# Kernel tuning notes

Measured on AMD Instinct MI355X. Metric: run time of the kernel, lower is better.

Reference implementation:

```python
import jax, jax.numpy as jnp
import numpy as np

DEPTH, HEADS, DIM_HEAD = 6, 12, 64
DIM, MLP, FEAT = 768, 3072, 1000
B, N = 32, 196
EPS = 1e-5


def layernorm(x, g, b):
    m = jnp.mean(x, axis=-1, keepdims=True)
    v = jnp.var(x, axis=-1, keepdims=True)
    return (x - m) * jax.lax.rsqrt(v + EPS) * g + b


def setup_inputs() -> dict:
    key = jax.random.key(0)
    ks = jax.random.split(key, 8)
    s = 0.02
    return {
        "x": jax.random.normal(ks[0], (B, N, DIM), jnp.float32),
        "cls_token": jax.random.normal(ks[1], (1, 1, DIM), jnp.float32),
        "ln1_g": jnp.ones((DEPTH, DIM), jnp.float32),
        "ln1_b": jnp.zeros((DEPTH, DIM), jnp.float32),
        "w_qkv": jax.random.normal(ks[2], (DEPTH, DIM, 3 * HEADS * DIM_HEAD), jnp.float32) * s,
        "reattn_w": jax.random.normal(ks[3], (DEPTH, HEADS, HEADS), jnp.float32),
        "reattn_g": jnp.ones((DEPTH, HEADS), jnp.float32),
        "reattn_b": jnp.zeros((DEPTH, HEADS), jnp.float32),
        "w_out": jax.random.normal(ks[4], (DEPTH, HEADS * DIM_HEAD, DIM), jnp.float32) * s,
        "b_out": jnp.zeros((DEPTH, DIM), jnp.float32),
        "ln2_g": jnp.ones((DEPTH, DIM), jnp.float32),
        "ln2_b": jnp.zeros((DEPTH, DIM), jnp.float32),
        "w1": jax.random.normal(ks[5], (DEPTH, DIM, MLP), jnp.float32) * s,
        "b1": jnp.zeros((DEPTH, MLP), jnp.float32),
        "w2": jax.random.normal(ks[6], (DEPTH, MLP, DIM), jnp.float32) * s,
        "b2": jnp.zeros((DEPTH, DIM), jnp.float32),
        "lnf_g": jnp.ones((DIM,), jnp.float32),
        "lnf_b": jnp.zeros((DIM,), jnp.float32),
        "w_head": jax.random.normal(ks[7], (DIM, FEAT), jnp.float32) * s,
        "b_head": jnp.zeros((FEAT,), jnp.float32),
    }


def _forward(x, cls_token, ln1_g, ln1_b, w_qkv, reattn_w, reattn_g, reattn_b,
             w_out, b_out, ln2_g, ln2_b, w1, b1, w2, b2, lnf_g, lnf_b, w_head, b_head):
    b = x.shape[0]
    cls = jnp.broadcast_to(cls_token, (b, 1, DIM))
    x = jnp.concatenate([cls, x], axis=1)  # (B, N+1, DIM)
    n = x.shape[1]
    scale = DIM_HEAD ** -0.5
    for l in range(DEPTH):
        h = layernorm(x, ln1_g[l], ln1_b[l])
        qkv = h @ w_qkv[l]                       # (B, n, 3*H*Dh)
        qkv = qkv.reshape(b, n, 3, HEADS, DIM_HEAD)
        q, k, v = (qkv[:, :, i].transpose(0, 2, 1, 3) for i in range(3))  # b h n d
        dots = jnp.einsum('bhid,bhjd->bhij', q, k) * scale
        attn = jax.nn.softmax(dots, axis=-1)
        attn = jnp.einsum('bhij,hg->bgij', attn, reattn_w[l])
        # per-head LayerNorm: normalize over head axis (axis=1)
        m = jnp.mean(attn, axis=1, keepdims=True)
        var = jnp.var(attn, axis=1, keepdims=True)
        attn = (attn - m) * jax.lax.rsqrt(var + EPS)
        attn = attn * reattn_g[l][None, :, None, None] + reattn_b[l][None, :, None, None]
        out = jnp.einsum('bhij,bhjd->bhid', attn, v)
        out = out.transpose(0, 2, 1, 3).reshape(b, n, HEADS * DIM_HEAD)
        x = x + out @ w_out[l] + b_out[l]
        h = layernorm(x, ln2_g[l], ln2_b[l])
        h = jax.nn.gelu(h @ w1[l] + b1[l], approximate=False)
        x = x + h @ w2[l] + b2[l]
    pooled = x[:, 0]  # cls pool
    return layernorm(pooled, lnf_g, lnf_b) @ w_head + b_head


def reference(x, cls_token, ln1_g, ln1_b, w_qkv, reattn_w, reattn_g, reattn_b,
              w_out, b_out, ln2_g, ln2_b, w1, b1, w2, b2, lnf_g, lnf_b, w_head, b_head):
    return _forward(x, cls_token, ln1_g, ln1_b, w_qkv, reattn_w, reattn_g, reattn_b,
                    w_out, b_out, ln2_g, ln2_b, w1, b1, w2, b2, lnf_g, lnf_b, w_head, b_head)
```

## Files before the change

### kernel.cpp

```cpp
#include <hip/hip_runtime.h>
#include <cstdint>

typedef __bf16 bf16_t;
typedef __bf16 bf16x8 __attribute__((ext_vector_type(8)));
typedef float  f32x4  __attribute__((ext_vector_type(4)));
typedef unsigned int u32;

#define DEPTH 6
#define HEADS 12
#define DH    64
#define DIM   768
#define MLPD  3072
#define FEAT  1000
#define BATCH 32
#define SEQ   197
#define NP    224
#define TOK   (BATCH*SEQ)

__device__ __forceinline__ f32x4 zero4() {
    f32x4 z; z[0] = 0.f; z[1] = 0.f; z[2] = 0.f; z[3] = 0.f; return z;
}

__device__ __forceinline__ f32x4 mfma16(bf16x8 a, bf16x8 b, f32x4 c) {
    return __builtin_amdgcn_mfma_f32_16x16x32_bf16(a, b, c, 0, 0, 0);
}

typedef const __attribute__((address_space(1))) u32* gas_ptr;
typedef __attribute__((address_space(3))) u32*       las_ptr;
__device__ __forceinline__ void gload16(const bf16_t* g, bf16_t* l) {
    __builtin_amdgcn_global_load_lds((gas_ptr)g, (las_ptr)l, 16, 0, 0);
}

__global__ __launch_bounds__(256) void concat_k(const float* __restrict__ x,
                                                const float* __restrict__ cls,
                                                float* __restrict__ xbuf) {
    int idx = blockIdx.x * 256 + threadIdx.x;
    int col = idx % DIM;
    int row = idx / DIM;
    int b = row / SEQ, p = row % SEQ;
    xbuf[idx] = (p == 0) ? cls[col] : x[(b * 196 + p - 1) * DIM + col];
}

__global__ __launch_bounds__(256) void tcvt_k(const float* __restrict__ W,
                                              bf16_t* __restrict__ Wt,
                                              int K, int N) {
    __shared__ float t[32][33];
    int n0 = blockIdx.x * 32, k0 = blockIdx.y * 32;
    int c = threadIdx.x & 31, r = threadIdx.x >> 5;
#pragma unroll
    for (int i = 0; i < 4; i++) {
        int k = k0 + r + i * 8, n = n0 + c;
        t[r + i * 8][c] = (n < N) ? W[k * N + n] : 0.f;
    }
    __syncthreads();
#pragma unroll
    for (int i = 0; i < 4; i++) {
        int n = n0 + r + i * 8, k = k0 + c;
        if (n < N) Wt[n * K + k] = (bf16_t)t[c][r + i * 8];
    }
}

__global__ __launch_bounds__(256) void ln_k(const float* __restrict__ x, long row_stride,
                                            const float* __restrict__ g,
                                            const float* __restrict__ b,
                                            bf16_t* __restrict__ out) {
    int row = blockIdx.x;
    const float* xr = x + (long)row * row_stride;
    int t = threadIdx.x;
    float v0 = xr[t], v1 = xr[t + 256], v2 = xr[t + 512];
    float s  = v0 + v1 + v2;
    float sq = v0 * v0 + v1 * v1 + v2 * v2;
#pragma unroll
    for (int o = 1; o < 64; o <<= 1) { s += __shfl_xor(s, o); sq += __shfl_xor(sq, o); }
    __shared__ float ss[4], sqs[4];
    int w = t >> 6;
    if ((t & 63) == 0) { ss[w] = s; sqs[w] = sq; }
    __syncthreads();
    s  = ss[0] + ss[1] + ss[2] + ss[3];
    sq = sqs[0] + sqs[1] + sqs[2] + sqs[3];
    float m  = s * (1.f / 768.f);
    float rs = rsqrtf(sq * (1.f / 768.f) - m * m + 1e-5f);
    bf16_t* orow = out + (long)row * DIM;
    orow[t]       = (bf16_t)((v0 - m) * rs * g[t]       + b[t]);
    orow[t + 256] = (bf16_t)((v1 - m) * rs * g[t + 256] + b[t + 256]);
    orow[t + 512] = (bf16_t)((v2 - m) * rs * g[t + 512] + b[t + 512]);
}

template <int MODE>
__global__ __launch_bounds__(256) void gemm_k(const bf16_t* __restrict__ A,
                                              const bf16_t* __restrict__ Bt,
                                              const float* __restrict__ bias,
                                              float* __restrict__ Cf,
                                              bf16_t* __restrict__ Cb,
                                              int M, int N, int K) {
    __shared__ bf16_t sA[2][128][32];
    __shared__ bf16_t sB[2][128][32];
    int tid = threadIdx.x;
    int bm = blockIdx.x * 128, bn = blockIdx.y * 128;
    int wave = tid >> 6, lane = tid & 63;
    int wm = (wave >> 1) * 64, wn = (wave & 1) * 64;
    int la = lane & 15, lb = lane >> 4;

    int rowA[2], rowB[2], colE[2];
#pragma unroll
    for (int q = 0; q < 2; q++) {
        int li = (wave * 2 + q) * 64 + lane;
        int row = li >> 2;
        colE[q] = (li & 3) * 8;
        int ar = bm + row; if (ar > M - 1) ar = M - 1;
        int br = bn + row; if (br > N - 1) br = N - 1;
        rowA[q] = ar; rowB[q] = br;
    }

    f32x4 acc[4][4];
#pragma unroll
    for (int m = 0; m < 4; m++)
#pragma unroll
        for (int n = 0; n < 4; n++) acc[m][n] = zero4();

    int nt = K >> 5;

#pragma unroll
    for (int q = 0; q < 2; q++) {
        gload16(A  + (long)rowA[q] * K + colE[q], &sA[0][0][0] + (wave * 2 + q) * 512);
        gload16(Bt + (long)rowB[q] * K + colE[q], &sB[0][0][0] + (wave * 2 + q) * 512);
    }
    __syncthreads();

    for (int t = 0; t < nt; t++) {
        int cur = t & 1;
        if (t + 1 < nt) {
            int k0 = (t + 1) << 5;
#pragma unroll
            for (int q = 0; q < 2; q++) {
                gload16(A  + (long)rowA[q] * K + k0 + colE[q], &sA[cur ^ 1][0][0] + (wave * 2 + q) * 512);
                gload16(Bt + (long)rowB[q] * K + k0 + colE[q], &sB[cur ^ 1][0][0] + (wave * 2 + q) * 512);
            }
        }
        bf16x8 af[4], bfr[4];
#pragma unroll
        for (int m = 0; m < 4; m++) af[m]  = *(const bf16x8*)&sA[cur][wm + m * 16 + la][lb * 8];
#pragma unroll
        for (int n = 0; n < 4; n++) bfr[n] = *(const bf16x8*)&sB[cur][wn + n * 16 + la][lb * 8];
#pragma unroll
        for (int m = 0; m < 4; m++)
#pragma unroll
            for (int n = 0; n < 4; n++)
                acc[m][n] = mfma16(af[m], bfr[n], acc[m][n]);
        __syncthreads();
    }

#pragma unroll
    for (int m = 0; m < 4; m++) {
#pragma unroll
        for (int n = 0; n < 4; n++) {
            int ib = bm + wm + m * 16 + lb * 4;
            int jb = bn + wn + n * 16 + la;
            if (jb >= N) continue;
            float bv = (MODE == 0) ? 0.f : bias[jb];
#pragma unroll
            for (int r = 0; r < 4; r++) {
                int i = ib + r;
                if (i >= M) continue;
                float v = acc[m][n][r];
                if (MODE == 0) {
                    Cb[(long)i * N + jb] = (bf16_t)v;
                } else if (MODE == 1) {
                    Cf[(long)i * N + jb] += v + bv;
                } else if (MODE == 2) {
                    float u = v + bv;
                    Cb[(long)i * N + jb] = (bf16_t)(0.5f * u * (1.f + erff(u * 0.70710678118f)));
                } else {
                    Cf[(long)i * N + jb] = v + bv;
                }
            }
        }
    }
}

__global__ __launch_bounds__(256) void qk_k(const bf16_t* __restrict__ qkv,
                                            float* __restrict__ dots) {
    int bh = blockIdx.z;
    int b = bh / HEADS, h = bh % HEADS;
    int i0 = blockIdx.x * 64, j0 = blockIdx.y * 64;
    __shared__ bf16_t sQ[64][32], sK[64][32];
    int tid = threadIdx.x, wave = tid >> 6, lane = tid & 63;
    int wm = (wave >> 1) * 32, wn = (wave & 1) * 32;
    int la = lane & 15, lb = lane >> 4;
    f32x4 acc[2][2];
#pragma unroll
    for (int m = 0; m < 2; m++)
#pragma unroll
        for (int n = 0; n < 2; n++) acc[m][n] = zero4();

    int row = tid >> 2, col = (tid & 3) * 8;
    int qi = i0 + row; if (qi > SEQ - 1) qi = SEQ - 1;
    int kj = j0 + row; if (kj > SEQ - 1) kj = SEQ - 1;
    const bf16_t* qsrc = qkv + (((b * SEQ + qi) * 3 + 0) * HEADS + h) * DH + col;
    const bf16_t* ksrc = qkv + (((b * SEQ + kj) * 3 + 1) * HEADS + h) * DH + col;

#pragma unroll
    for (int d0 = 0; d0 < 64; d0 += 32) {
        *(bf16x8*)&sQ[row][col] = *(const bf16x8*)(qsrc + d0);
        *(bf16x8*)&sK[row][col] = *(const bf16x8*)(ksrc + d0);
        __syncthreads();
        bf16x8 af[2], bfr[2];
#pragma unroll
        for (int m = 0; m < 2; m++) af[m]  = *(const bf16x8*)&sQ[wm + m * 16 + la][lb * 8];
#pragma unroll
        for (int n = 0; n < 2; n++) bfr[n] = *(const bf16x8*)&sK[wn + n * 16 + la][lb * 8];
#pragma unroll
        for (int m = 0; m < 2; m++)
#pragma unroll
            for (int n = 0; n < 2; n++)
                acc[m][n] = mfma16(af[m], bfr[n], acc[m][n]);
        __syncthreads();
    }
#pragma unroll
    for (int m = 0; m < 2; m++)
#pragma unroll
        for (int n = 0; n < 2; n++)
#pragma unroll
            for (int r = 0; r < 4; r++) {
                int i = i0 + wm + m * 16 + lb * 4 + r;
                int j = j0 + wn + n * 16 + la;
                if (i < SEQ && j < SEQ)
                    dots[((long)bh * SEQ + i) * NP + j] = acc[m][n][r] * 0.125f;
            }
}

__global__ __launch_bounds__(256) void smre_k(const float* __restrict__ dots,
                                              const float* __restrict__ W,
                                              const float* __restrict__ gg,
                                              const float* __restrict__ bb,
                                              bf16_t* __restrict__ attn2) {
    __shared__ float sm[HEADS][NP];
    __shared__ float sW[HEADS * HEADS];
    __shared__ float sg[HEADS], sb[HEADS];
    int tid = threadIdx.x;
    if (tid < HEADS * HEADS) sW[tid] = W[tid];
    if (tid < HEADS) { sg[tid] = gg[tid]; sb[tid] = bb[tid]; }
    int bi = blockIdx.x;
    int b = bi / SEQ, i = bi % SEQ;
    int wave = tid >> 6, lane = tid & 63;

    for (int h = wave; h < HEADS; h += 4) {
        const float* p = dots + ((long)(b * HEADS + h) * SEQ + i) * NP;
        float v[4], e[4];
#pragma unroll
        for (int q = 0; q < 4; q++) { int j = lane + 64 * q; v[q] = (j < SEQ) ? p[j] : -3.0e38f; }
        float mx = fmaxf(fmaxf(v[0], v[1]), fmaxf(v[2], v[3]));
#pragma unroll
        for (int o = 1; o < 64; o <<= 1) mx = fmaxf(mx, __shfl_xor(mx, o));
        float s = 0.f;
#pragma unroll
        for (int q = 0; q < 4; q++) {
            int j = lane + 64 * q;
            e[q] = (j < SEQ) ? __expf(v[q] - mx) : 0.f;
            s += e[q];
        }
#pragma unroll
        for (int o = 1; o < 64; o <<= 1) s += __shfl_xor(s, o);
        float inv = 1.f / s;
#pragma unroll
        for (int q = 0; q < 4; q++) { int j = lane + 64 * q; if (j < NP) sm[h][j] = e[q] * inv; }
    }
    __syncthreads();

    int j = tid;
    if (j >= NP) return;
    bool valid = j < SEQ;
    float vals[HEADS];
#pragma unroll
    for (int h = 0; h < HEADS; h++) vals[h] = valid ? sm[h][j] : 0.f;
    float mix[HEADS];
    float s = 0.f, sq = 0.f;
#pragma unroll
    for (int g = 0; g < HEADS; g++) {
        float a = 0.f;
#pragma unroll
        for (int h = 0; h < HEADS; h++) a += vals[h] * sW[h * HEADS + g];
        mix[g] = a; s += a; sq += a * a;
    }
    float m  = s * (1.f / 12.f);
    float rs = rsqrtf(sq * (1.f / 12.f) - m * m + 1e-5f);
    long base = ((long)(b * HEADS) * SEQ + i) * NP + j;
    const long hs = (long)SEQ * NP;
#pragma unroll
    for (int g = 0; g < HEADS; g++) {
        float o = valid ? ((mix[g] - m) * rs * sg[g] + sb[g]) : 0.f;
        attn2[base + g * hs] = (bf16_t)o;
    }
}

__global__ __launch_bounds__(256) void pv_k(const bf16_t* __restrict__ attn2,
                                            const bf16_t* __restrict__ qkv,
                                            bf16_t* __restrict__ aout) {
    int bh = blockIdx.y;
    int b = bh / HEADS, h = bh % HEADS;
    int i0 = blockIdx.x * 64;
    __shared__ bf16_t sP[64][32];
    __shared__ bf16_t sVt[64][32];
    int tid = threadIdx.x, wave = tid >> 6, lane = tid & 63;
    int wm = (wave >> 1) * 32, wn = (wave & 1) * 32;
    int la = lane & 15, lb = lane >> 4;
    f32x4 acc[2][2];
#pragma unroll
    for (int m = 0; m < 2; m++)
#pragma unroll
        for (int n = 0; n < 2; n++) acc[m][n] = zero4();

    int prow = tid >> 2, pcol = (tid & 3) * 8;
    int pi = i0 + prow; if (pi > SEQ - 1) pi = SEQ - 1;
    const bf16_t* psrc = attn2 + ((long)bh * SEQ + pi) * NP + pcol;
    int jl = tid >> 3, dblk = (tid & 7) * 8;
    int jlx = jl ^ ((tid & 3) << 3);

    for (int j0 = 0; j0 < NP; j0 += 32) {
        *(bf16x8*)&sP[prow][pcol] = *(const bf16x8*)(psrc + j0);
        int jg = j0 + jl;
        bf16x8 vv;
#pragma unroll
        for (int e = 0; e < 8; e++) vv[e] = (bf16_t)0.f;
        if (jg < SEQ)
            vv = *(const bf16x8*)(qkv + (((b * SEQ + jg) * 3 + 2) * HEADS + h) * DH + dblk);
#pragma unroll
        for (int e = 0; e < 8; e++) sVt[dblk + e][jlx] = vv[e];
        __syncthreads();
        bf16x8 af[2], bfr[2];
#pragma unroll
        for (int m = 0; m < 2; m++) af[m] = *(const bf16x8*)&sP[wm + m * 16 + la][lb * 8];
#pragma unroll
        for (int n = 0; n < 2; n++) {
            int rowd = wn + n * 16 + la;
            int colj = (lb * 8) ^ (((rowd >> 3) & 3) << 3);
            bfr[n] = *(const bf16x8*)&sVt[rowd][colj];
        }
#pragma unroll
        for (int m = 0; m < 2; m++)
#pragma unroll
            for (int n = 0; n < 2; n++)
                acc[m][n] = mfma16(af[m], bfr[n], acc[m][n]);
        __syncthreads();
    }
#pragma unroll
    for (int m = 0; m < 2; m++)
#pragma unroll
        for (int n = 0; n < 2; n++)
#pragma unroll
            for (int r = 0; r < 4; r++) {
                int i = i0 + wm + m * 16 + lb * 4 + r;
                int d = wn + n * 16 + la;
                if (i < SEQ)
                    aout[((long)b * SEQ + i) * DIM + h * DH + d] = (bf16_t)acc[m][n][r];
            }
}

extern "C" void kernel_launch(void* const* d_in, const int* in_sizes, int n_in,
                              void* d_out, int out_size, void* d_ws, size_t ws_size,
                              hipStream_t stream) {
    const float* x        = (const float*)d_in[0];
    const float* cls      = (const float*)d_in[1];
    const float* ln1_g    = (const float*)d_in[2];
    const float* ln1_b    = (const float*)d_in[3];
    const float* w_qkv    = (const float*)d_in[4];
    const float* reattn_w = (const float*)d_in[5];
    const float* reattn_g = (const float*)d_in[6];
    const float* reattn_b = (const float*)d_in[7];
    const float* w_out    = (const float*)d_in[8];
    const float* b_out    = (const float*)d_in[9];
    const float* ln2_g    = (const float*)d_in[10];
    const float* ln2_b    = (const float*)d_in[11];
    const float* w1       = (const float*)d_in[12];
    const float* b1       = (const float*)d_in[13];
    const float* w2       = (const float*)d_in[14];
    const float* b2       = (const float*)d_in[15];
    const float* lnf_g    = (const float*)d_in[16];
    const float* lnf_b    = (const float*)d_in[17];
    const float* w_head   = (const float*)d_in[18];
    const float* b_head   = (const float*)d_in[19];
    float* out = (float*)d_out;

    char* p = (char*)d_ws;
    auto alloc = [&](size_t bytes) -> char* {
        char* r = p;
        p += (bytes + 255) & ~(size_t)255;
        return r;
    };
    bf16_t* wt      = (bf16_t*)alloc(2ULL * MLPD * DIM);
    bf16_t* wt_head = (bf16_t*)alloc(2ULL * FEAT * DIM);
    float*  xbuf    = (float*)alloc(4ULL * TOK * DIM);
    bf16_t* h_ln    = (bf16_t*)alloc(2ULL * TOK * DIM);
    bf16_t* qkv     = (bf16_t*)alloc(2ULL * TOK * 3 * DIM);
    float*  dots    = (float*)alloc(4ULL * BATCH * HEADS * SEQ * NP);
    bf16_t* h_mid   = (bf16_t*)dots;
    bf16_t* attn2   = (bf16_t*)alloc(2ULL * BATCH * HEADS * SEQ * NP);
    bf16_t* aout    = (bf16_t*)alloc(2ULL * TOK * DIM);

    dim3 B256(256);
    concat_k<<<(TOK * DIM) / 256, B256, 0, stream>>>(x, cls, xbuf);
    tcvt_k<<<dim3((FEAT + 31) / 32, DIM / 32), B256, 0, stream>>>(w_head, wt_head, DIM, FEAT);

    for (int l = 0; l < DEPTH; l++) {
        ln_k<<<TOK, B256, 0, stream>>>(xbuf, DIM, ln1_g + l * DIM, ln1_b + l * DIM, h_ln);
        tcvt_k<<<dim3(2304 / 32, DIM / 32), B256, 0, stream>>>(w_qkv + (long)l * DIM * 2304, wt, DIM, 2304);
        gemm_k<0><<<dim3(50, 18), B256, 0, stream>>>(h_ln, wt, nullptr, nullptr, qkv, TOK, 2304, DIM);
        qk_k<<<dim3(4, 4, BATCH * HEADS), B256, 0, stream>>>(qkv, dots);
        smre_k<<<TOK, B256, 0, stream>>>(
            dots, reattn_w + l * HEADS * HEADS, reattn_g + l * HEADS, reattn_b + l * HEADS, attn2);
        pv_k<<<dim3(4, BATCH * HEADS), B256, 0, stream>>>(attn2, qkv, aout);
        tcvt_k<<<dim3(DIM / 32, DIM / 32), B256, 0, stream>>>(w_out + (long)l * DIM * DIM, wt, DIM, DIM);
        gemm_k<1><<<dim3(50, 6), B256, 0, stream>>>(aout, wt, b_out + l * DIM, xbuf, nullptr, TOK, DIM, DIM);
        ln_k<<<TOK, B256, 0, stream>>>(xbuf, DIM, ln2_g + l * DIM, ln2_b + l * DIM, h_ln);
        tcvt_k<<<dim3(MLPD / 32, DIM / 32), B256, 0, stream>>>(w1 + (long)l * DIM * MLPD, wt, DIM, MLPD);
        gemm_k<2><<<dim3(50, 24), B256, 0, stream>>>(h_ln, wt, b1 + l * MLPD, nullptr, h_mid, TOK, MLPD, DIM);
        tcvt_k<<<dim3(DIM / 32, MLPD / 32), B256, 0, stream>>>(w2 + (long)l * MLPD * DIM, wt, MLPD, DIM);
        gemm_k<1><<<dim3(50, 6), B256, 0, stream>>>(h_mid, wt, b2 + l * DIM, xbuf, nullptr, TOK, DIM, MLPD);
    }

    ln_k<<<BATCH, B256, 0, stream>>>(xbuf, (long)SEQ * DIM, lnf_g, lnf_b, h_ln);
    gemm_k<3><<<dim3(1, 8), B256, 0, stream>>>(h_ln, wt_head, b_head, out, nullptr, BATCH, FEAT, DIM);
}
```

Baseline: 2.143 ms.

## Add 256x128 triple-buffered swizzled GEMM kernel for transformer layer matmuls

Replaces the 128x128 double-buffered GEMM with a new 512-thread kernel that computes 256x128 tiles with a BK=64 k-step. Shared memory is triple-buffered and loads are tracked with explicit vmcnt waits, and the LDS layout is XOR-swizzled to avoid bank conflicts. MFMA sections are raised with s_setprio. The aim is more data reuse per block, better overlap of global loads with compute, and fewer stalls. In exchange it uses more LDS and registers, and the larger M tiles waste more work on the padded edge since TOK=6304 is not a multiple of 256. The final head GEMM keeps the old kernel as a specialised bias-store version.

Result: slower. 2.251 ms (+5.0%).

```diff
diff --git a/kernel.cpp b/kernel.cpp
--- a/kernel.cpp
+++ b/kernel.cpp
@@ -87,11 +87,120 @@
 }
 
 template <int MODE>
-__global__ __launch_bounds__(256) void gemm_k(const bf16_t* __restrict__ A,
+__global__ __launch_bounds__(512, 2) void gemm2_k(const bf16_t* __restrict__ A,
+                                                  const bf16_t* __restrict__ Bt,
+                                                  const float* __restrict__ bias,
+                                                  float* __restrict__ Cf,
+                                                  bf16_t* __restrict__ Cb,
+                                                  int M, int N, int K) {
+    __shared__ bf16_t sA[3][256 * 64];
+    __shared__ bf16_t sB[3][128 * 64];
+    int tid = threadIdx.x;
+    int bm = blockIdx.x * 256, bn = blockIdx.y * 128;
+    int wave = tid >> 6, lane = tid & 63;
+    int wm = (wave >> 1) * 64, wn = (wave & 1) * 64;
+    int la = lane & 15, lb = lane >> 4;
+
+    int trow = tid >> 3;
+    int sub  = ((tid & 7) ^ (trow & 7)) * 8;
+    int rA[4];
+#pragma unroll
+    for (int i = 0; i < 4; i++) {
+        int r = bm + i * 64 + trow;
+        rA[i] = (r < M) ? r : M - 1;
+    }
+    const bf16_t* Bbase = Bt + (long)bn * K;
+
+    f32x4 acc[4][4];
+#pragma unroll
+    for (int m = 0; m < 4; m++)
+#pragma unroll
+        for (int n = 0; n < 4; n++) acc[m][n] = zero4();
+
+    int NT = K >> 6;
+
+    auto stage = [&](int buf, int kt) {
+        int k0 = kt << 6;
+#pragma unroll
+        for (int i = 0; i < 4; i++)
+            gload16(A + (long)rA[i] * K + k0 + sub, &sA[buf][0] + i * 4096 + wave * 512);
+#pragma unroll
+        for (int i = 0; i < 2; i++)
+            gload16(Bbase + (long)(i * 64 + trow) * K + k0 + sub, &sB[buf][0] + i * 4096 + wave * 512);
+    };
+
+    int coff0 = ((0 * 32 + lb * 8) ^ ((la & 7) << 3));
+    int coff1 = ((1 * 32 + lb * 8) ^ ((la & 7) << 3));
+
+    stage(0, 0);
+    stage(1, 1);
+    asm volatile("s_waitcnt vmcnt(6)" ::: "memory");
+    __builtin_amdgcn_s_barrier();
+    asm volatile("" ::: "memory");
+
+    for (int t = 0; t < NT; t++) {
+        int c = t % 3;
+        bool pf = (t + 2) < NT;
+        if (pf) stage((t + 2) % 3, t + 2);
+
+        const bf16_t* cA = &sA[c][0];
+        const bf16_t* cB = &sB[c][0];
+        bf16x8 af[4][2], bf[4][2];
+#pragma unroll
+        for (int m = 0; m < 4; m++) {
+            int row = (wm + m * 16 + la) * 64;
+            af[m][0] = *(const bf16x8*)(cA + row + coff0);
+            af[m][1] = *(const bf16x8*)(cA + row + coff1);
+        }
+#pragma unroll
+        for (int n = 0; n < 4; n++) {
+            int row = (wn + n * 16 + la) * 64;
+            bf[n][0] = *(const bf16x8*)(cB + row + coff0);
+            bf[n][1] = *(const bf16x8*)(cB + row + coff1);
+        }
+        __builtin_amdgcn_s_setprio(1);
+#pragma unroll
+        for (int m = 0; m < 4; m++)
+#pragma unroll
+            for (int n = 0; n < 4; n++)
+                acc[m][n] = mfma16(af[m][1], bf[n][1], mfma16(af[m][0], bf[n][0], acc[m][n]));
+        __builtin_amdgcn_s_setprio(0);
+
+        if (pf) asm volatile("s_waitcnt vmcnt(6)" ::: "memory");
+        else    asm volatile("s_waitcnt vmcnt(0)" ::: "memory");
+        __builtin_amdgcn_s_barrier();
+        asm volatile("" ::: "memory");
+    }
+
+#pragma unroll
+    for (int m = 0; m < 4; m++) {
+#pragma unroll
+        for (int n = 0; n < 4; n++) {
+            int ib = bm + wm + m * 16 + lb * 4;
+            int jb = bn + wn + n * 16 + la;
+            float bv = (MODE == 0) ? 0.f : bias[jb];
+#pragma unroll
+            for (int r = 0; r < 4; r++) {
+                int i = ib + r;
+                if (i >= M) continue;
+                float v = acc[m][n][r];
+                if (MODE == 0) {
+                    Cb[(long)i * N + jb] = (bf16_t)v;
+                } else if (MODE == 1) {
+                    Cf[(long)i * N + jb] += v + bv;
+                } else {
+                    float u = v + bv;
+                    Cb[(long)i * N + jb] = (bf16_t)(0.5f * u * (1.f + erff(u * 0.70710678118f)));
+                }
+            }
+        }
+    }
+}
+
+__global__ __launch_bounds__(256) void gemm_s(const bf16_t* __restrict__ A,
                                               const bf16_t* __restrict__ Bt,
                                               const float* __restrict__ bias,
                                               float* __restrict__ Cf,
-                                              bf16_t* __restrict__ Cb,
                                               int M, int N, int K) {
     __shared__ bf16_t sA[2][128][32];
     __shared__ bf16_t sB[2][128][32];
@@ -100,7 +209,6 @@
     int wave = tid >> 6, lane = tid & 63;
     int wm = (wave >> 1) * 64, wn = (wave & 1) * 64;
     int la = lane & 15, lb = lane >> 4;
-
     int rowA[2], rowB[2], colE[2];
 #pragma unroll
     for (int q = 0; q < 2; q++) {
@@ -111,22 +219,18 @@
         int br = bn + row; if (br > N - 1) br = N - 1;
         rowA[q] = ar; rowB[q] = br;
     }
-
     f32x4 acc[4][4];
 #pragma unroll
     for (int m = 0; m < 4; m++)
 #pragma unroll
         for (int n = 0; n < 4; n++) acc[m][n] = zero4();
-
     int nt = K >> 5;
-
 #pragma unroll
     for (int q = 0; q < 2; q++) {
         gload16(A  + (long)rowA[q] * K + colE[q], &sA[0][0][0] + (wave * 2 + q) * 512);
         gload16(Bt + (long)rowB[q] * K + colE[q], &sB[0][0][0] + (wave * 2 + q) * 512);
     }
     __syncthreads();
-
     for (int t = 0; t < nt; t++) {
         int cur = t & 1;
         if (t + 1 < nt) {
@@ -149,7 +253,6 @@
                 acc[m][n] = mfma16(af[m], bfr[n], acc[m][n]);
         __syncthreads();
     }
-
 #pragma unroll
     for (int m = 0; m < 4; m++) {
 #pragma unroll
@@ -157,22 +260,12 @@
             int ib = bm + wm + m * 16 + lb * 4;
             int jb = bn + wn + n * 16 + la;
             if (jb >= N) continue;
-            float bv = (MODE == 0) ? 0.f : bias[jb];
+            float bv = bias[jb];
 #pragma unroll
             for (int r = 0; r < 4; r++) {
                 int i = ib + r;
                 if (i >= M) continue;
-                float v = acc[m][n][r];
-                if (MODE == 0) {
-                    Cb[(long)i * N + jb] = (bf16_t)v;
-                } else if (MODE == 1) {
-                    Cf[(long)i * N + jb] += v + bv;
-                } else if (MODE == 2) {
-                    float u = v + bv;
-                    Cb[(long)i * N + jb] = (bf16_t)(0.5f * u * (1.f + erff(u * 0.70710678118f)));
-                } else {
-                    Cf[(long)i * N + jb] = v + bv;
-                }
+                Cf[(long)i * N + jb] = acc[m][n][r] + bv;
             }
         }
     }
@@ -397,27 +490,28 @@
     bf16_t* attn2   = (bf16_t*)alloc(2ULL * BATCH * HEADS * SEQ * NP);
     bf16_t* aout    = (bf16_t*)alloc(2ULL * TOK * DIM);
 
-    dim3 B256(256);
+    dim3 B256(256), B512(512);
+    const int GX = (TOK + 255) / 256;
     concat_k<<<(TOK * DIM) / 256, B256, 0, stream>>>(x, cls, xbuf);
     tcvt_k<<<dim3((FEAT + 31) / 32, DIM / 32), B256, 0, stream>>>(w_head, wt_head, DIM, FEAT);
 
     for (int l = 0; l < DEPTH; l++) {
         ln_k<<<TOK, B256, 0, stream>>>(xbuf, DIM, ln1_g + l * DIM, ln1_b + l * DIM, h_ln);
         tcvt_k<<<dim3(2304 / 32, DIM / 32), B256, 0, stream>>>(w_qkv + (long)l * DIM * 2304, wt, DIM, 2304);
-        gemm_k<0><<<dim3(50, 18), B256, 0, stream>>>(h_ln, wt, nullptr, nullptr, qkv, TOK, 2304, DIM);
+        gemm2_k<0><<<dim3(GX, 18), B512, 0, stream>>>(h_ln, wt, nullptr, nullptr, qkv, TOK, 2304, DIM);
         qk_k<<<dim3(4, 4, BATCH * HEADS), B256, 0, stream>>>(qkv, dots);
         smre_k<<<TOK, B256, 0, stream>>>(
             dots, reattn_w + l * HEADS * HEADS, reattn_g + l * HEADS, reattn_b + l * HEADS, attn2);
         pv_k<<<dim3(4, BATCH * HEADS), B256, 0, stream>>>(attn2, qkv, aout);
         tcvt_k<<<dim3(DIM / 32, DIM / 32), B256, 0, stream>>>(w_out + (long)l * DIM * DIM, wt, DIM, DIM);
-        gemm_k<1><<<dim3(50, 6), B256, 0, stream>>>(aout, wt, b_out + l * DIM, xbuf, nullptr, TOK, DIM, DIM);
+        gemm2_k<1><<<dim3(GX, 6), B512, 0, stream>>>(aout, wt, b_out + l * DIM, xbuf, nullptr, TOK, DIM, DIM);
         ln_k<<<TOK, B256, 0, stream>>>(xbuf, DIM, ln2_g + l * DIM, ln2_b + l * DIM, h_ln);
         tcvt_k<<<dim3(MLPD / 32, DIM / 32), B256, 0, stream>>>(w1 + (long)l * DIM * MLPD, wt, DIM, MLPD);
-        gemm_k<2><<<dim3(50, 24), B256, 0, stream>>>(h_ln, wt, b1 + l * MLPD, nullptr, h_mid, TOK, MLPD, DIM);
+        gemm2_k<2><<<dim3(GX, 24), B512, 0, stream>>>(h_ln, wt, b1 + l * MLPD, nullptr, h_mid, TOK, MLPD, DIM);
         tcvt_k<<<dim3(DIM / 32, MLPD / 32), B256, 0, stream>>>(w2 + (long)l * MLPD * DIM, wt, MLPD, DIM);
-        gemm_k<1><<<dim3(50, 6), B256, 0, stream>>>(h_mid, wt, b2 + l * DIM, xbuf, nullptr, TOK, DIM, MLPD);
+        gemm2_k<1><<<dim3(GX, 6), B512, 0, stream>>>(h_mid, wt, b2 + l * DIM, xbuf, nullptr, TOK, DIM, MLPD);
     }
 
     ln_k<<<BATCH, B256, 0, stream>>>(xbuf, (long)SEQ * DIM, lnf_g, lnf_b, h_ln);
-    gemm_k<3><<<dim3(1, 8), B256, 0, stream>>>(h_ln, wt_head, b_head, out, nullptr, BATCH, FEAT, DIM);
-}
+    gemm_s<<<dim3(1, 8), B256, 0, stream>>>(h_ln, wt_head, b_head, out, BATCH, FEAT, DIM);
+}
```

## Replace GEMMs with triple-buffered, swizzled, XCD-aware tiled kernels

Applied to the files above, without the earlier changes.

Replaces the generic double-buffered GEMM with two specialized kernels. The wide-N GEMMs (QKV, MLP1) use a 256x256 tile with 512 threads, and the narrow-N ones (out-proj, MLP2) use a 128x128 tile. Both use triple-buffered global-to-LDS loads with explicit vmcnt waits, one barrier per k-step, XOR-swizzled LDS layout to avoid bank conflicts, setprio around MFMA bursts, and XCD-aware block remapping for L2 locality. The aim is to hide memory latency and raise MFMA utilization, at the cost of more LDS and register pressure plus fragile hand-written waitcnt logic.

Result: slower. 2.511 ms (+17.2%).

```diff
diff --git a/kernel.cpp b/kernel.cpp
--- a/kernel.cpp
+++ b/kernel.cpp
@@ -29,6 +29,11 @@
 typedef __attribute__((address_space(3))) u32*       las_ptr;
 __device__ __forceinline__ void gload16(const bf16_t* g, bf16_t* l) {
     __builtin_amdgcn_global_load_lds((gas_ptr)g, (las_ptr)l, 16, 0, 0);
+}
+
+__device__ __forceinline__ int xcd_logical(int L, int nblk) {
+    int q = nblk >> 3, r = nblk & 7, xcd = L & 7;
+    return (xcd < r ? xcd * (q + 1) : r * (q + 1) + (xcd - r) * q) + (L >> 3);
 }
 
 __global__ __launch_bounds__(256) void concat_k(const float* __restrict__ x,
@@ -87,11 +92,219 @@
 }
 
 template <int MODE>
-__global__ __launch_bounds__(256) void gemm_k(const bf16_t* __restrict__ A,
+__global__ __launch_bounds__(512, 2) void gemmN_k(const bf16_t* __restrict__ A,
+                                                  const bf16_t* __restrict__ Bt,
+                                                  const float* __restrict__ bias,
+                                                  bf16_t* __restrict__ Cb,
+                                                  int M, int N, int K, int nN) {
+    __shared__ bf16_t sA[3][256 * 32];
+    __shared__ bf16_t sB[3][256 * 32];
+    int tid = threadIdx.x;
+    int g = xcd_logical(blockIdx.x, gridDim.x);
+    int bm = (g / nN) * 256, bn = (g % nN) * 256;
+
+    int wave = tid >> 6, lane = tid & 63;
+    int wm = (wave >> 2) * 128, wn = (wave & 3) * 64;
+    int la = lane & 15, lb = lane >> 4;
+
+    int trow = tid >> 2;
+    int sub  = ((tid & 3) ^ (trow & 3)) * 8;
+    int rA[2], rB[2];
+#pragma unroll
+    for (int i = 0; i < 2; i++) {
+        int rr = bm + i * 128 + trow; rA[i] = (rr < M) ? rr : M - 1;
+        rB[i] = bn + i * 128 + trow;
+    }
+    int coff = (lb * 8) ^ ((la & 3) << 3);
+
+    f32x4 acc[8][4];
+#pragma unroll
+    for (int m = 0; m < 8; m++)
+#pragma unroll
+        for (int n = 0; n < 4; n++) acc[m][n] = zero4();
+
+    int NT = K >> 5;
+
+    auto stageA = [&](int buf, int k0) {
+#pragma unroll
+        for (int i = 0; i < 2; i++)
+            gload16(A + (long)rA[i] * K + k0 + sub, &sA[buf][0] + i * 4096 + wave * 512);
+    };
+    auto stageB = [&](int buf, int k0) {
+#pragma unroll
+        for (int i = 0; i < 2; i++)
+            gload16(Bt + (long)rB[i] * K + k0 + sub, &sB[buf][0] + i * 4096 + wave * 512);
+    };
+
+    stageA(0, 0);  stageB(0, 0);
+    stageA(1, 32); stageB(1, 32);
+
+    for (int t = 0; t < NT; t++) {
+        int bt = t % 3, bs = (t + 2) % 3;
+        int kst = (t + 2) << 5;
+        bool st = (t + 2) < NT;
+        if (t + 1 < NT) asm volatile("s_waitcnt vmcnt(4)" ::: "memory");
+        else            asm volatile("s_waitcnt vmcnt(0)" ::: "memory");
+        __builtin_amdgcn_s_barrier();
+        __builtin_amdgcn_sched_barrier(0);
+
+        const bf16_t* cA = &sA[bt][0];
+        const bf16_t* cB = &sB[bt][0];
+        bf16x8 bv[4];
+#pragma unroll
+        for (int nf = 0; nf < 4; nf++)
+            bv[nf] = *(const bf16x8*)(cB + (wn + nf * 16 + la) * 32 + coff);
+
+        if (st) stageA(bs, kst);
+        bf16x8 av[4];
+#pragma unroll
+        for (int mf = 0; mf < 4; mf++)
+            av[mf] = *(const bf16x8*)(cA + (wm + mf * 16 + la) * 32 + coff);
+        asm volatile("s_waitcnt lgkmcnt(0)" ::: "memory");
+        __builtin_amdgcn_sched_barrier(0);
+        __builtin_amdgcn_s_setprio(1);
+#pragma unroll
+        for (int mf = 0; mf < 4; mf++)
+#pragma unroll
+            for (int nf = 0; nf < 4; nf++)
+                acc[mf][nf] = mfma16(av[mf], bv[nf], acc[mf][nf]);
+        __builtin_amdgcn_s_setprio(0);
+        __builtin_amdgcn_sched_barrier(0);
+
+        if (st) stageB(bs, kst);
+#pragma unroll
+        for (int mf = 0; mf < 4; mf++)
+            av[mf] = *(const bf16x8*)(cA + (wm + 64 + mf * 16 + la) * 32 + coff);
+        asm volatile("s_waitcnt lgkmcnt(0)" ::: "memory");
+        __builtin_amdgcn_sched_barrier(0);
+        __builtin_amdgcn_s_setprio(1);
+#pragma unroll
+        for (int mf = 0; mf < 4; mf++)
+#pragma unroll
+            for (int nf = 0; nf < 4; nf++)
+                acc[4 + mf][nf] = mfma16(av[mf], bv[nf], acc[4 + mf][nf]);
+        __builtin_amdgcn_s_setprio(0);
+    }
+
+#pragma unroll
+    for (int mi = 0; mi < 8; mi++) {
+#pragma unroll
+        for (int nf = 0; nf < 4; nf++) {
+            int ib = bm + wm + mi * 16 + lb * 4;
+            int jb = bn + wn + nf * 16 + la;
+            float bvv = (MODE == 0) ? 0.f : bias[jb];
+#pragma unroll
+            for (int rr = 0; rr < 4; rr++) {
+                int i = ib + rr;
+                if (i >= M) continue;
+                float v = acc[mi][nf][rr];
+                if (MODE == 0) {
+                    Cb[(long)i * N + jb] = (bf16_t)v;
+                } else {
+                    float u = v + bvv;
+                    Cb[(long)i * N + jb] = (bf16_t)(0.5f * u * (1.f + erff(u * 0.70710678118f)));
+                }
+            }
+        }
+    }
+}
+
+__global__ __launch_bounds__(256, 4) void gemmS_k(const bf16_t* __restrict__ A,
+                                                  const bf16_t* __restrict__ Bt,
+                                                  const float* __restrict__ bias,
+                                                  float* __restrict__ Cf,
+                                                  int M, int N, int K, int nN) {
+    __shared__ bf16_t sA[3][128 * 32];
+    __shared__ bf16_t sB[3][128 * 32];
+    int tid = threadIdx.x;
+    int g = xcd_logical(blockIdx.x, gridDim.x);
+    int bm = (g / nN) * 128, bn = (g % nN) * 128;
+
+    int wave = tid >> 6, lane = tid & 63;
+    int wm = (wave >> 1) * 64, wn = (wave & 1) * 64;
+    int la = lane & 15, lb = lane >> 4;
+
+    int trow = tid >> 2;
+    int sub  = ((tid & 3) ^ (trow & 3)) * 8;
+    int rA[2], rB[2];
+#pragma unroll
+    for (int i = 0; i < 2; i++) {
+        int rr = bm + i * 64 + trow; rA[i] = (rr < M) ? rr : M - 1;
+        rB[i] = bn + i * 64 + trow;
+    }
+    int coff = (lb * 8) ^ ((la & 3) << 3);
+
+    f32x4 acc[4][4];
+#pragma unroll
+    for (int m = 0; m < 4; m++)
+#pragma unroll
+        for (int n = 0; n < 4; n++) acc[m][n] = zero4();
+
+    int NT = K >> 5;
+
+    auto stage = [&](int buf, int k0) {
+#pragma unroll
+        for (int i = 0; i < 2; i++)
+            gload16(A + (long)rA[i] * K + k0 + sub, &sA[buf][0] + i * 2048 + wave * 512);
+#pragma unroll
+        for (int i = 0; i < 2; i++)
+            gload16(Bt + (long)rB[i] * K + k0 + sub, &sB[buf][0] + i * 2048 + wave * 512);
+    };
+
+    stage(0, 0);
+    stage(1, 32);
+
+    for (int t = 0; t < NT; t++) {
+        int bt = t % 3, bs = (t + 2) % 3;
+        bool st = (t + 2) < NT;
+        if (t + 1 < NT) asm volatile("s_waitcnt vmcnt(4)" ::: "memory");
+        else            asm volatile("s_waitcnt vmcnt(0)" ::: "memory");
+        __builtin_amdgcn_s_barrier();
+        __builtin_amdgcn_sched_barrier(0);
+
+        if (st) stage(bs, (t + 2) << 5);
+
+        const bf16_t* cA = &sA[bt][0];
+        const bf16_t* cB = &sB[bt][0];
+        bf16x8 av[4], bv[4];
+#pragma unroll
+        for (int mf = 0; mf < 4; mf++)
+            av[mf] = *(const bf16x8*)(cA + (wm + mf * 16 + la) * 32 + coff);
+#pragma unroll
+        for (int nf = 0; nf < 4; nf++)
+            bv[nf] = *(const bf16x8*)(cB + (wn + nf * 16 + la) * 32 + coff);
+        asm volatile("s_waitcnt lgkmcnt(0)" ::: "memory");
+        __builtin_amdgcn_sched_barrier(0);
+        __builtin_amdgcn_s_setprio(1);
+#pragma unroll
+        for (int mf = 0; mf < 4; mf++)
+#pragma unroll
+            for (int nf = 0; nf < 4; nf++)
+                acc[mf][nf] = mfma16(av[mf], bv[nf], acc[mf][nf]);
+        __builtin_amdgcn_s_setprio(0);
+    }
+
+#pragma unroll
+    for (int mf = 0; mf < 4; mf++) {
+#pragma unroll
+        for (int nf = 0; nf < 4; nf++) {
+            int ib = bm + wm + mf * 16 + lb * 4;
+            int jb = bn + wn + nf * 16 + la;
+            float bvv = bias[jb];
+#pragma unroll
+            for (int rr = 0; rr < 4; rr++) {
+                int i = ib + rr;
+                if (i >= M) continue;
+                Cf[(long)i * N + jb] += acc[mf][nf][rr] + bvv;
+            }
+        }
+    }
+}
+
+__global__ __launch_bounds__(256) void gemm_h(const bf16_t* __restrict__ A,
                                               const bf16_t* __restrict__ Bt,
                                               const float* __restrict__ bias,
                                               float* __restrict__ Cf,
-                                              bf16_t* __restrict__ Cb,
                                               int M, int N, int K) {
     __shared__ bf16_t sA[2][128][32];
     __shared__ bf16_t sB[2][128][32];
@@ -100,7 +313,6 @@
     int wave = tid >> 6, lane = tid & 63;
     int wm = (wave >> 1) * 64, wn = (wave & 1) * 64;
     int la = lane & 15, lb = lane >> 4;
-
     int rowA[2], rowB[2], colE[2];
 #pragma unroll
     for (int q = 0; q < 2; q++) {
@@ -111,22 +323,18 @@
         int br = bn + row; if (br > N - 1) br = N - 1;
         rowA[q] = ar; rowB[q] = br;
     }
-
     f32x4 acc[4][4];
 #pragma unroll
     for (int m = 0; m < 4; m++)
 #pragma unroll
         for (int n = 0; n < 4; n++) acc[m][n] = zero4();
-
     int nt = K >> 5;
-
 #pragma unroll
     for (int q = 0; q < 2; q++) {
         gload16(A  + (long)rowA[q] * K + colE[q], &sA[0][0][0] + (wave * 2 + q) * 512);
         gload16(Bt + (long)rowB[q] * K + colE[q], &sB[0][0][0] + (wave * 2 + q) * 512);
     }
     __syncthreads();
-
     for (int t = 0; t < nt; t++) {
         int cur = t & 1;
         if (t + 1 < nt) {
@@ -149,7 +357,6 @@
                 acc[m][n] = mfma16(af[m], bfr[n], acc[m][n]);
         __syncthreads();
     }
-
 #pragma unroll
     for (int m = 0; m < 4; m++) {
 #pragma unroll
@@ -157,22 +364,12 @@
             int ib = bm + wm + m * 16 + lb * 4;
             int jb = bn + wn + n * 16 + la;
             if (jb >= N) continue;
-            float bv = (MODE == 0) ? 0.f : bias[jb];
+            float bv = bias[jb];
 #pragma unroll
             for (int r = 0; r < 4; r++) {
                 int i = ib + r;
                 if (i >= M) continue;
-                float v = acc[m][n][r];
-                if (MODE == 0) {
-                    Cb[(long)i * N + jb] = (bf16_t)v;
-                } else if (MODE == 1) {
-                    Cf[(long)i * N + jb] += v + bv;
-                } else if (MODE == 2) {
-                    float u = v + bv;
-                    Cb[(long)i * N + jb] = (bf16_t)(0.5f * u * (1.f + erff(u * 0.70710678118f)));
-                } else {
-                    Cf[(long)i * N + jb] = v + bv;
-                }
+                Cf[(long)i * N + jb] = acc[m][n][r] + bv;
             }
         }
     }
@@ -397,27 +594,29 @@
     bf16_t* attn2   = (bf16_t*)alloc(2ULL * BATCH * HEADS * SEQ * NP);
     bf16_t* aout    = (bf16_t*)alloc(2ULL * TOK * DIM);
 
-    dim3 B256(256);
+    dim3 B256(256), B512(512);
+    const int NM256 = (TOK + 255) / 256;
+    const int NM128 = (TOK + 127) / 128;
     concat_k<<<(TOK * DIM) / 256, B256, 0, stream>>>(x, cls, xbuf);
     tcvt_k<<<dim3((FEAT + 31) / 32, DIM / 32), B256, 0, stream>>>(w_head, wt_head, DIM, FEAT);
 
     for (int l = 0; l < DEPTH; l++) {
         ln_k<<<TOK, B256, 0, stream>>>(xbuf, DIM, ln1_g + l * DIM, ln1_b + l * DIM, h_ln);
         tcvt_k<<<dim3(2304 / 32, DIM / 32), B256, 0, stream>>>(w_qkv + (long)l * DIM * 2304, wt, DIM, 2304);
-        gemm_k<0><<<dim3(50, 18), B256, 0, stream>>>(h_ln, wt, nullptr, nullptr, qkv, TOK, 2304, DIM);
+        gemmN_k<0><<<NM256 * 9, B512, 0, stream>>>(h_ln, wt, nullptr, qkv, TOK, 2304, DIM, 9);
         qk_k<<<dim3(4, 4, BATCH * HEADS), B256, 0, stream>>>(qkv, dots);
         smre_k<<<TOK, B256, 0, stream>>>(
             dots, reattn_w + l * HEADS * HEADS, reattn_g + l * HEADS, reattn_b + l * HEADS, attn2);
         pv_k<<<dim3(4, BATCH * HEADS), B256, 0, stream>>>(attn2, qkv, aout);
         tcvt_k<<<dim3(DIM / 32, DIM / 32), B256, 0, stream>>>(w_out + (long)l * DIM * DIM, wt, DIM, DIM);
-        gemm_k<1><<<dim3(50, 6), B256, 0, stream>>>(aout, wt, b_out + l * DIM, xbuf, nullptr, TOK, DIM, DIM);
+        gemmS_k<<<NM128 * 6, B256, 0, stream>>>(aout, wt, b_out + l * DIM, xbuf, TOK, DIM, DIM, 6);
         ln_k<<<TOK, B256, 0, stream>>>(xbuf, DIM, ln2_g + l * DIM, ln2_b + l * DIM, h_ln);
         tcvt_k<<<dim3(MLPD / 32, DIM / 32), B256, 0, stream>>>(w1 + (long)l * DIM * MLPD, wt, DIM, MLPD);
-        gemm_k<2><<<dim3(50, 24), B256, 0, stream>>>(h_ln, wt, b1 + l * MLPD, nullptr, h_mid, TOK, MLPD, DIM);
+        gemmN_k<2><<<NM256 * 12, B512, 0, stream>>>(h_ln, wt, b1 + l * MLPD, h_mid, TOK, MLPD, DIM, 12);
         tcvt_k<<<dim3(DIM / 32, MLPD / 32), B256, 0, stream>>>(w2 + (long)l * MLPD * DIM, wt, MLPD, DIM);
-        gemm_k<1><<<dim3(50, 6), B256, 0, stream>>>(h_mid, wt, b2 + l * DIM, xbuf, nullptr, TOK, DIM, MLPD);
+        gemmS_k<<<NM128 * 6, B256, 0, stream>>>(h_mid, wt, b2 + l * DIM, xbuf, TOK, DIM, MLPD, 6);
     }
 
     ln_k<<<BATCH, B256, 0, stream>>>(xbuf, (long)SEQ * DIM, lnf_g, lnf_b, h_ln);
-    gemm_k<3><<<dim3(1, 8), B256, 0, stream>>>(h_ln, wt_head, b_head, out, nullptr, BATCH, FEAT, DIM);
-}
+    gemm_h<<<dim3(1, 8), B256, 0, stream>>>(h_ln, wt_head, b_head, out, BATCH, FEAT, DIM);
+}
```

## Triple-buffer GEMM with XCD-aware block mapping and swizzled LDS

Applied to the files above, without the earlier changes.

Rewrites the main transformer GEMM kernel to use a three-stage LDS ring with explicit vmcnt waits and a single barrier per k-step, so global loads run two tiles ahead of the MFMA work. It adds an XOR swizzle on LDS columns to reduce bank conflicts, maps a 1D grid onto XCD-contiguous tile ranges for L2 locality, sets wave priority around the MFMA block and requests 3 blocks per CU. The head projection moves to a separate kernel that keeps the old bounds checks. The cost is higher LDS use and register pressure, and the N-boundary check is dropped on the assumption that all N values are multiples of 128.

Measured after the change: 2.068 ms. 3.5% less time.

```diff
diff --git a/kernel.cpp b/kernel.cpp
--- a/kernel.cpp
+++ b/kernel.cpp
@@ -29,6 +29,11 @@
 typedef __attribute__((address_space(3))) u32*       las_ptr;
 __device__ __forceinline__ void gload16(const bf16_t* g, bf16_t* l) {
     __builtin_amdgcn_global_load_lds((gas_ptr)g, (las_ptr)l, 16, 0, 0);
+}
+
+__device__ __forceinline__ int xcd_logical(int L, int nblk) {
+    int q = nblk >> 3, r = nblk & 7, xcd = L & 7;
+    return (xcd < r ? xcd * (q + 1) : r * (q + 1) + (xcd - r) * q) + (L >> 3);
 }
 
 __global__ __launch_bounds__(256) void concat_k(const float* __restrict__ x,
@@ -87,11 +92,106 @@
 }
 
 template <int MODE>
-__global__ __launch_bounds__(256) void gemm_k(const bf16_t* __restrict__ A,
+__global__ __launch_bounds__(256, 3) void gemm_k(const bf16_t* __restrict__ A,
+                                                 const bf16_t* __restrict__ Bt,
+                                                 const float* __restrict__ bias,
+                                                 float* __restrict__ Cf,
+                                                 bf16_t* __restrict__ Cb,
+                                                 int M, int N, int K, int nN) {
+    __shared__ bf16_t sA[3][128 * 32];
+    __shared__ bf16_t sB[3][128 * 32];
+    bf16_t* sa = &sA[0][0];
+    bf16_t* sb = &sB[0][0];
+    int tid = threadIdx.x;
+    int g = xcd_logical(blockIdx.x, gridDim.x);
+    int bm = (g / nN) * 128, bn = (g % nN) * 128;
+    int wave = tid >> 6, lane = tid & 63;
+    int wm = (wave >> 1) * 64, wn = (wave & 1) * 64;
+    int la = lane & 15, lb = lane >> 4;
+
+    int tq = tid >> 2;
+    int scol = ((tid & 3) ^ ((tid >> 3) & 3)) * 8;
+    int a0 = bm + tq;      if (a0 > M - 1) a0 = M - 1;
+    int a1 = bm + 64 + tq; if (a1 > M - 1) a1 = M - 1;
+    int b0 = bn + tq, b1 = bn + 64 + tq;
+    int wslot = wave * 512;
+
+    int lbx = (lb ^ ((la >> 1) & 3)) << 3;
+
+    f32x4 acc[4][4];
+#pragma unroll
+    for (int m = 0; m < 4; m++)
+#pragma unroll
+        for (int n = 0; n < 4; n++) acc[m][n] = zero4();
+
+    int NT = K >> 5;
+
+    auto stage = [&](int buf, int kt) {
+        int k0 = kt << 5;
+        gload16(A  + (long)a0 * K + k0 + scol, sa + buf * 4096 + wslot);
+        gload16(A  + (long)a1 * K + k0 + scol, sa + buf * 4096 + 2048 + wslot);
+        gload16(Bt + (long)b0 * K + k0 + scol, sb + buf * 4096 + wslot);
+        gload16(Bt + (long)b1 * K + k0 + scol, sb + buf * 4096 + 2048 + wslot);
+    };
+
+    stage(0, 0);
+    stage(1, 1);
+
+    for (int t = 0; t < NT; t++) {
+        if (t < NT - 1) asm volatile("s_waitcnt vmcnt(4)" ::: "memory");
+        else            asm volatile("s_waitcnt vmcnt(0)" ::: "memory");
+        __builtin_amdgcn_s_barrier();
+        asm volatile("" ::: "memory");
+
+        if (t + 2 < NT) stage((t + 2) % 3, t + 2);
+
+        const bf16_t* cA = sa + (t % 3) * 4096;
+        const bf16_t* cB = sb + (t % 3) * 4096;
+        bf16x8 av[4], bv[4];
+#pragma unroll
+        for (int mf = 0; mf < 4; mf++)
+            av[mf] = *(const bf16x8*)(cA + (wm + mf * 16 + la) * 32 + lbx);
+#pragma unroll
+        for (int nf = 0; nf < 4; nf++)
+            bv[nf] = *(const bf16x8*)(cB + (wn + nf * 16 + la) * 32 + lbx);
+        __builtin_amdgcn_s_setprio(1);
+#pragma unroll
+        for (int mf = 0; mf < 4; mf++)
+#pragma unroll
+            for (int nf = 0; nf < 4; nf++)
+                acc[mf][nf] = mfma16(av[mf], bv[nf], acc[mf][nf]);
+        __builtin_amdgcn_s_setprio(0);
+    }
+
+#pragma unroll
+    for (int mf = 0; mf < 4; mf++) {
+#pragma unroll
+        for (int nf = 0; nf < 4; nf++) {
+            int ib = bm + wm + mf * 16 + lb * 4;
+            int jb = bn + wn + nf * 16 + la;
+            float bvv = (MODE == 0) ? 0.f : bias[jb];
+#pragma unroll
+            for (int rr = 0; rr < 4; rr++) {
+                int i = ib + rr;
+                if (i >= M) continue;
+                float v = acc[mf][nf][rr];
+                if (MODE == 0) {
+                    Cb[(long)i * N + jb] = (bf16_t)v;
+                } else if (MODE == 1) {
+                    Cf[(long)i * N + jb] += v + bvv;
+                } else {
+                    float u = v + bvv;
+                    Cb[(long)i * N + jb] = (bf16_t)(0.5f * u * (1.f + erff(u * 0.70710678118f)));
+                }
+            }
+        }
+    }
+}
+
+__global__ __launch_bounds__(256) void gemm_h(const bf16_t* __restrict__ A,
                                               const bf16_t* __restrict__ Bt,
                                               const float* __restrict__ bias,
                                               float* __restrict__ Cf,
-                                              bf16_t* __restrict__ Cb,
                                               int M, int N, int K) {
     __shared__ bf16_t sA[2][128][32];
     __shared__ bf16_t sB[2][128][32];
@@ -100,7 +200,6 @@
     int wave = tid >> 6, lane = tid & 63;
     int wm = (wave >> 1) * 64, wn = (wave & 1) * 64;
     int la = lane & 15, lb = lane >> 4;
-
     int rowA[2], rowB[2], colE[2];
 #pragma unroll
     for (int q = 0; q < 2; q++) {
@@ -111,22 +210,18 @@
         int br = bn + row; if (br > N - 1) br = N - 1;
         rowA[q] = ar; rowB[q] = br;
     }
-
     f32x4 acc[4][4];
 #pragma unroll
     for (int m = 0; m < 4; m++)
 #pragma unroll
         for (int n = 0; n < 4; n++) acc[m][n] = zero4();
-
     int nt = K >> 5;
-
 #pragma unroll
     for (int q = 0; q < 2; q++) {
         gload16(A  + (long)rowA[q] * K + colE[q], &sA[0][0][0] + (wave * 2 + q) * 512);
         gload16(Bt + (long)rowB[q] * K + colE[q], &sB[0][0][0] + (wave * 2 + q) * 512);
     }
     __syncthreads();
-
     for (int t = 0; t < nt; t++) {
         int cur = t & 1;
         if (t + 1 < nt) {
@@ -149,7 +244,6 @@
                 acc[m][n] = mfma16(af[m], bfr[n], acc[m][n]);
         __syncthreads();
     }
-
 #pragma unroll
     for (int m = 0; m < 4; m++) {
 #pragma unroll
@@ -157,22 +251,12 @@
             int ib = bm + wm + m * 16 + lb * 4;
             int jb = bn + wn + n * 16 + la;
             if (jb >= N) continue;
-            float bv = (MODE == 0) ? 0.f : bias[jb];
+            float bv = bias[jb];
 #pragma unroll
             for (int r = 0; r < 4; r++) {
                 int i = ib + r;
                 if (i >= M) continue;
-                float v = acc[m][n][r];
-                if (MODE == 0) {
-                    Cb[(long)i * N + jb] = (bf16_t)v;
-                } else if (MODE == 1) {
-                    Cf[(long)i * N + jb] += v + bv;
-                } else if (MODE == 2) {
-                    float u = v + bv;
-                    Cb[(long)i * N + jb] = (bf16_t)(0.5f * u * (1.f + erff(u * 0.70710678118f)));
-                } else {
-                    Cf[(long)i * N + jb] = v + bv;
-                }
+                Cf[(long)i * N + jb] = acc[m][n][r] + bv;
             }
         }
     }
@@ -398,26 +482,27 @@
     bf16_t* aout    = (bf16_t*)alloc(2ULL * TOK * DIM);
 
     dim3 B256(256);
+    const int NM = (TOK + 127) / 128;
     concat_k<<<(TOK * DIM) / 256, B256, 0, stream>>>(x, cls, xbuf);
     tcvt_k<<<dim3((FEAT + 31) / 32, DIM / 32), B256, 0, stream>>>(w_head, wt_head, DIM, FEAT);
 
     for (int l = 0; l < DEPTH; l++) {
         ln_k<<<TOK, B256, 0, stream>>>(xbuf, DIM, ln1_g + l * DIM, ln1_b + l * DIM, h_ln);
         tcvt_k<<<dim3(2304 / 32, DIM / 32), B256, 0, stream>>>(w_qkv + (long)l * DIM * 2304, wt, DIM, 2304);
-        gemm_k<0><<<dim3(50, 18), B256, 0, stream>>>(h_ln, wt, nullptr, nullptr, qkv, TOK, 2304, DIM);
+        gemm_k<0><<<NM * 18, B256, 0, stream>>>(h_ln, wt, nullptr, nullptr, qkv, TOK, 2304, DIM, 18);
         qk_k<<<dim3(4, 4, BATCH * HEADS), B256, 0, stream>>>(qkv, dots);
         smre_k<<<TOK, B256, 0, stream>>>(
             dots, reattn_w + l * HEADS * HEADS, reattn_g + l * HEADS, reattn_b + l * HEADS, attn2);
         pv_k<<<dim3(4, BATCH * HEADS), B256, 0, stream>>>(attn2, qkv, aout);
         tcvt_k<<<dim3(DIM / 32, DIM / 32), B256, 0, stream>>>(w_out + (long)l * DIM * DIM, wt, DIM, DIM);
-        gemm_k<1><<<dim3(50, 6), B256, 0, stream>>>(aout, wt, b_out + l * DIM, xbuf, nullptr, TOK, DIM, DIM);
+        gemm_k<1><<<NM * 6, B256, 0, stream>>>(aout, wt, b_out + l * DIM, xbuf, nullptr, TOK, DIM, DIM, 6);
         ln_k<<<TOK, B256, 0, stream>>>(xbuf, DIM, ln2_g + l * DIM, ln2_b + l * DIM, h_ln);
         tcvt_k<<<dim3(MLPD / 32, DIM / 32), B256, 0, stream>>>(w1 + (long)l * DIM * MLPD, wt, DIM, MLPD);
-        gemm_k<2><<<dim3(50, 24), B256, 0, stream>>>(h_ln, wt, b1 + l * MLPD, nullptr, h_mid, TOK, MLPD, DIM);
+        gemm_k<2><<<NM * 24, B256, 0, stream>>>(h_ln, wt, b1 + l * MLPD, nullptr, h_mid, TOK, MLPD, DIM, 24);
         tcvt_k<<<dim3(DIM / 32, MLPD / 32), B256, 0, stream>>>(w2 + (long)l * MLPD * DIM, wt, MLPD, DIM);
-        gemm_k<1><<<dim3(50, 6), B256, 0, stream>>>(h_mid, wt, b2 + l * DIM, xbuf, nullptr, TOK, DIM, MLPD);
+        gemm_k<1><<<NM * 6, B256, 0, stream>>>(h_mid, wt, b2 + l * DIM, xbuf, nullptr, TOK, DIM, MLPD, 6);
     }
 
     ln_k<<<BATCH, B256, 0, stream>>>(xbuf, (long)SEQ * DIM, lnf_g, lnf_b, h_ln);
-    gemm_k<3><<<dim3(1, 8), B256, 0, stream>>>(h_ln, wt_head, b_head, out, nullptr, BATCH, FEAT, DIM);
-}
+    gemm_h<<<dim3(1, 8), B256, 0, stream>>>(h_ln, wt_head, b_head, out, BATCH, FEAT, DIM);
+}
```
